# Optimization experiments

Measured on AMD Instinct MI355X. Metric: run time of the kernel, lower is better.

Reference implementation:

```python
import jax, jax.numpy as jnp
import numpy as np
import math

JOINT_DIM = 16
D_MODEL = 128
NUM_HEADS = 8
HEAD_DIM = D_MODEL // NUM_HEADS


def kinematic_adjacency():
    adj = np.zeros((JOINT_DIM, JOINT_DIM), dtype=np.float32)
    skeleton = [(0, 1), (1, 2), (2, 3), (0, 4), (4, 5), (5, 6), (0, 7), (7, 8),
                (8, 9), (0, 10), (10, 11), (11, 12), (0, 13), (13, 14), (14, 15)]
    for p, c in skeleton:
        adj[p, c] = 1.0
        adj[c, p] = 1.0
    sym = [(4, 7), (5, 8), (6, 9), (10, 13), (11, 14), (12, 15)]
    for a, b in sym:
        adj[a, b] += 0.8
        adj[b, a] += 0.8
    adj += np.eye(JOINT_DIM, dtype=np.float32)
    return jnp.asarray(adj)


def setup_inputs() -> dict:
    key = jax.random.key(0)
    ks = jax.random.split(key, 9)
    B, S = 64, 512
    s3 = 1.0 / math.sqrt(3.0)
    sd = 1.0 / math.sqrt(D_MODEL)
    return {
        "x": jax.random.normal(ks[0], (B, S, JOINT_DIM, 3), dtype=jnp.float32),
        "Wq": jax.random.uniform(ks[1], (3, D_MODEL), jnp.float32, -s3, s3),
        "bq": jax.random.uniform(ks[2], (D_MODEL,), jnp.float32, -s3, s3),
        "Wk": jax.random.uniform(ks[3], (3, D_MODEL), jnp.float32, -s3, s3),
        "bk": jax.random.uniform(ks[4], (D_MODEL,), jnp.float32, -s3, s3),
        "Wv": jax.random.uniform(ks[5], (3, D_MODEL), jnp.float32, -s3, s3),
        "bv": jax.random.uniform(ks[6], (D_MODEL,), jnp.float32, -s3, s3),
        "Wo": jax.random.uniform(ks[7], (D_MODEL, D_MODEL), jnp.float32, -sd, sd),
        "bo": jax.random.uniform(ks[8], (D_MODEL,), jnp.float32, -sd, sd),
    }


def reference(x, Wq, bq, Wk, bk, Wv, bv, Wo, bo):
    B, S, J, _ = x.shape
    adj = kinematic_adjacency()  # [J, J]

    def split_heads(t):  # [B,S,J,D] -> [B,S,H,J,hd]
        return t.reshape(B, S, J, NUM_HEADS, HEAD_DIM).transpose(0, 1, 3, 2, 4)

    q = split_heads(x @ Wq + bq)
    k = split_heads(x @ Wk + bk)
    v = split_heads(x @ Wv + bv)

    # scores get adjacency bias BEFORE the 1/sqrt(head_dim) scaling (as in source)
    scores = jnp.einsum('bshjd,bshkd->bshjk', q, k)
    scores = (scores + adj) / math.sqrt(HEAD_DIM)
    w = jax.nn.softmax(scores, axis=-1)  # dropout inactive (eval)
    ctx = jnp.einsum('bshjk,bshkd->bshjd', w, v)
    ctx = ctx.transpose(0, 1, 3, 2, 4).reshape(B, S, J, D_MODEL)
    return ctx @ Wo + bo  # [B,S,J,D]
```

## Files before the change

kernel.cpp:

```cpp
#include <hip/hip_runtime.h>

#define NJ   16
#define DM   128
#define NH   8
#define P    8
#define CL   0.36067376022224085f

typedef __attribute__((ext_vector_type(8))) short bf16x8;
typedef __attribute__((ext_vector_type(4))) float f32x4;

__constant__ float c_adj[NJ * NJ] = {
    1,1,0,0, 1,0,0,1, 0,0,1,0, 0,1,0,0,
    1,1,1,0, 0,0,0,0, 0,0,0,0, 0,0,0,0,
    0,1,1,1, 0,0,0,0, 0,0,0,0, 0,0,0,0,
    0,0,1,1, 0,0,0,0, 0,0,0,0, 0,0,0,0,
    1,0,0,0, 1,1,0,0.8f, 0,0,0,0, 0,0,0,0,
    0,0,0,0, 1,1,1,0, 0.8f,0,0,0, 0,0,0,0,
    0,0,0,0, 0,1,1,0, 0,0.8f,0,0, 0,0,0,0,
    1,0,0,0, 0.8f,0,0,1, 1,0,0,0, 0,0,0,0,
    0,0,0,0, 0,0.8f,0,1, 1,1,0,0, 0,0,0,0,
    0,0,0,0, 0,0,0.8f,0, 1,1,0,0, 0,0,0,0,
    1,0,0,0, 0,0,0,0, 0,0,1,1, 0,0.8f,0,0,
    0,0,0,0, 0,0,0,0, 0,0,1,1, 1,0,0.8f,0,
    0,0,0,0, 0,0,0,0, 0,0,0,1, 1,0,0,0.8f,
    1,0,0,0, 0,0,0,0, 0,0,0.8f,0, 0,1,1,0,
    0,0,0,0, 0,0,0,0, 0,0,0,0.8f, 0,1,1,1,
    0,0,0,0, 0,0,0,0, 0,0,0,0, 0.8f,0,1,1
};

#define WS_BP_W   0
#define WS_PACK_W 128
#define WS_GF_W   256

__device__ __forceinline__ unsigned short f2bf(float f) {
    union { float f; unsigned u; } v; v.f = f;
    unsigned u = v.u;
    u += 0x7FFFu + ((u >> 16) & 1u);
    return (unsigned short)(u >> 16);
}
__device__ __forceinline__ unsigned pack2bf(float lo, float hi) {
    return (unsigned)f2bf(lo) | ((unsigned)f2bf(hi) << 16);
}

__global__ __launch_bounds__(256) void skel_setup_kernel(
    const float* __restrict__ Wq, const float* __restrict__ bq,
    const float* __restrict__ Wk, const float* __restrict__ bk,
    const float* __restrict__ Wv, const float* __restrict__ bv,
    const float* __restrict__ Wo, const float* __restrict__ bo,
    unsigned* __restrict__ wsu)
{
    const int b = blockIdx.x, t = threadIdx.x;
    float* wsf = (float*)wsu;

    if (b < 8) {
        const int idx = b * 256 + t;
        const int ctl = idx >> 2, i = idx & 3;
        const int ct = ctl >> 6, l = ctl & 63;
        const int n  = ct * 16 + (l & 15);
        const int kb = (l >> 4) * 8;
        float v[2];
#pragma unroll
        for (int s = 0; s < 2; ++s) {
            const int k = kb + 2 * i + s;
            const int h = k >> 2, r = k & 3;
            float acc = 0.f;
            if (r < 3) {
#pragma unroll
                for (int dh = 0; dh < 16; ++dh)
                    acc += Wv[r * DM + h * 16 + dh] * Wo[(h * 16 + dh) * DM + n];
            }
            v[s] = acc;
        }
        wsu[WS_GF_W + idx] = pack2bf(v[0], v[1]);
        return;
    }
    if (t < 128) {
        const int n = t;
        float bv_ = bo[n];
        for (int d = 0; d < DM; ++d) bv_ += bv[d] * Wo[d * DM + n];
        wsf[WS_BP_W + n] = bv_;
    } else if (t < 128 + NH) {
        const int h = t - 128;
        float* o = &wsf[WS_PACK_W + h * 16];
#pragma unroll
        for (int r = 0; r < 3; ++r)
#pragma unroll
            for (int c = 0; c < 3; ++c) {
                float acc = 0.f;
#pragma unroll
                for (int dh = 0; dh < 16; ++dh)
                    acc += Wq[r * DM + h * 16 + dh] * Wk[c * DM + h * 16 + dh];
                o[r * 3 + c] = acc * CL;
            }
#pragma unroll
        for (int r = 0; r < 3; ++r) {
            float aa = 0.f, cc = 0.f;
#pragma unroll
            for (int dh = 0; dh < 16; ++dh) {
                aa += Wq[r * DM + h * 16 + dh] * bk[h * 16 + dh];
                cc += Wk[r * DM + h * 16 + dh] * bq[h * 16 + dh];
            }
            o[9 + r]  = aa * CL;
            o[12 + r] = cc * CL;
        }
        float dd = 0.f;
#pragma unroll
        for (int dh = 0; dh < 16; ++dh) dd += bq[h * 16 + dh] * bk[h * 16 + dh];
        o[15] = dd * CL;
    }
}

__global__ __launch_bounds__(256) void skel_main_kernel(
    const float* __restrict__ x,
    const unsigned* __restrict__ wsu,
    float* __restrict__ out,
    int npos)
{
    const int t = threadIdx.x;
    const long pos0 = (long)blockIdx.x * P;
    const float* wsf = (const float*)wsu;

    __shared__ __align__(16) float    sx4[P][NJ][4];
    __shared__ float                  sc[128];
    __shared__ __align__(16) float    st[4][NH][17][4];
    __shared__ __align__(16) unsigned sxb[4][NJ * 16];
    __shared__ __align__(16) unsigned sgf[2048];
    __shared__ __align__(16) float    sbp[128];

    if (t < 128) {
        const int p = t >> 4, j = t & 15;
        const long pidx = pos0 + p;
        const long base = pidx * 48 + j * 3;
        const bool ok = pidx < npos;
        sx4[p][j][0] = ok ? x[base + 0] : 0.f;
        sx4[p][j][1] = ok ? x[base + 1] : 0.f;
        sx4[p][j][2] = ok ? x[base + 2] : 0.f;
        sx4[p][j][3] = 0.f;
    } else {
        const int i = t - 128;
        sc[i]  = wsf[WS_PACK_W + i];
        sbp[i] = wsf[WS_BP_W + i];
    }
    {
        const uint4* gsrc = (const uint4*)&wsu[WS_GF_W];
        uint4* gdst = (uint4*)sgf;
        gdst[t]       = gsrc[t];
        gdst[t + 256] = gsrc[t + 256];
    }
    __syncthreads();

    const int wv = t >> 6, l = t & 63;
    const int h  = l >> 3, j0 = l & 7;

    float m[16];
#pragma unroll
    for (int i = 0; i < 16; ++i) m[i] = sc[h * 16 + i];
    float adj0[NJ], adj1[NJ];
#pragma unroll
    for (int k = 0; k < NJ; ++k) {
        adj0[k] = c_adj[j0 * NJ + k] * CL;
        adj1[k] = c_adj[(j0 + 8) * NJ + k] * CL;
    }

    const int jB = l & 15, lkB = l >> 4;

    for (int it = 0; it < 2; ++it) {
        const int p = wv * 2 + it;

        const f32x4 xa = *(const f32x4*)&sx4[p][j0];
        const f32x4 xb = *(const f32x4*)&sx4[p][j0 + 8];
        {
            f32x4 tv;
            tv.x = m[0]*xa.x + m[1]*xa.y + m[2]*xa.z;
            tv.y = m[3]*xa.x + m[4]*xa.y + m[5]*xa.z;
            tv.z = m[6]*xa.x + m[7]*xa.y + m[8]*xa.z;
            tv.w = m[12]*xa.x + m[13]*xa.y + m[14]*xa.z + m[15];
            *(f32x4*)&st[wv][h][j0][0] = tv;
            tv.x = m[0]*xb.x + m[1]*xb.y + m[2]*xb.z;
            tv.y = m[3]*xb.x + m[4]*xb.y + m[5]*xb.z;
            tv.z = m[6]*xb.x + m[7]*xb.y + m[8]*xb.z;
            tv.w = m[12]*xb.x + m[13]*xb.y + m[14]*xb.z + m[15];
            *(f32x4*)&st[wv][h][j0 + 8][0] = tv;
        }

        const float u0 = m[9]*xa.x + m[10]*xa.y + m[11]*xa.z;
        const float u1 = m[9]*xb.x + m[10]*xb.y + m[11]*xb.z;
        float sum0 = 0.f, sum1 = 0.f;
        float a00 = 0.f, a01 = 0.f, a02 = 0.f;
        float a10 = 0.f, a11 = 0.f, a12 = 0.f;
#pragma unroll
        for (int k = 0; k < NJ; ++k) {
            const f32x4 tk = *(const f32x4*)&st[wv][h][k][0];
            const f32x4 xk = *(const f32x4*)&sx4[p][k];
            const float s0 = xa.x*tk.x + xa.y*tk.y + xa.z*tk.z + (tk.w + u0 + adj0[k]);
            const float s1 = xb.x*tk.x + xb.y*tk.y + xb.z*tk.z + (tk.w + u1 + adj1[k]);
            const float e0 = exp2f(s0);
            const float e1 = exp2f(s1);
            sum0 += e0; sum1 += e1;
            a00 += e0 * xk.x; a01 += e0 * xk.y; a02 += e0 * xk.z;
            a10 += e1 * xk.x; a11 += e1 * xk.y; a12 += e1 * xk.z;
        }
        const float inv0 = __builtin_amdgcn_rcpf(sum0);
        const float inv1 = __builtin_amdgcn_rcpf(sum1);

        {
            uint2 w0, w1;
            w0.x = pack2bf(a00 * inv0, a01 * inv0);
            w0.y = pack2bf(a02 * inv0, 0.f);
            w1.x = pack2bf(a10 * inv1, a11 * inv1);
            w1.y = pack2bf(a12 * inv1, 0.f);
            *(uint2*)&sxb[wv][j0 * 16 + 2 * h]       = w0;
            *(uint2*)&sxb[wv][(j0 + 8) * 16 + 2 * h] = w1;
        }

        if (pos0 + p < npos) {
            const bf16x8 bvec = *(const bf16x8*)&sxb[wv][jB * 16 + lkB * 4];
            float* obase = out + (pos0 + p) * (long)(NJ * DM) + jB * DM + lkB * 4;
#pragma unroll
            for (int ct = 0; ct < 8; ++ct) {
                const bf16x8 ga = *(const bf16x8*)&sgf[(ct * 64 + l) * 4];
                const f32x4 bp4 = *(const f32x4*)&sbp[ct * 16 + lkB * 4];
                f32x4 acc = bp4;
                acc = __builtin_amdgcn_mfma_f32_16x16x32_bf16(ga, bvec, acc, 0, 0, 0);
                *(f32x4*)(obase + ct * 16) = acc;
            }
        }
    }
}

extern "C" void kernel_launch(void* const* d_in, const int* in_sizes, int n_in,
                              void* d_out, int out_size, void* d_ws, size_t ws_size,
                              hipStream_t stream) {
    const float* x  = (const float*)d_in[0];
    const float* Wq = (const float*)d_in[1];
    const float* bq = (const float*)d_in[2];
    const float* Wk = (const float*)d_in[3];
    const float* bk = (const float*)d_in[4];
    const float* Wv = (const float*)d_in[5];
    const float* bv = (const float*)d_in[6];
    const float* Wo = (const float*)d_in[7];
    const float* bo = (const float*)d_in[8];
    float* out    = (float*)d_out;
    unsigned* wsu = (unsigned*)d_ws;

    const int npos = in_sizes[0] / (NJ * 3);
    skel_setup_kernel<<<9, 256, 0, stream>>>(Wq, bq, Wk, bk, Wv, bv, Wo, bo, wsu);
    const int grid = (npos + P - 1) / P;
    skel_main_kernel<<<grid, 256, 0, stream>>>(x, wsu, out, npos);
}
```

Before: 78.66 us.

## Stage MFMA output through swizzled LDS for coalesced stores; keep weights in registers

Each wave now writes its MFMA results into a per-wave LDS tile using an XOR swizzle, then reads them back so each global store covers contiguous 1 KB rows instead of scattered 16-byte fragments. The projected weight fragments move from a per-block LDS copy into registers loaded straight from global memory. The per-head score transform is folded into per-query coefficients instead of going through an LDS staging table. This is meant to improve write coalescing on an output-bandwidth-bound kernel, at the cost of more LDS traffic, extra registers and a larger LDS footprint.

```diff
diff --git a/kernel.cpp b/kernel.cpp
--- a/kernel.cpp
+++ b/kernel.cpp
@@ -122,10 +122,9 @@
 
     __shared__ __align__(16) float    sx4[P][NJ][4];
     __shared__ float                  sc[128];
-    __shared__ __align__(16) float    st[4][NH][17][4];
-    __shared__ __align__(16) unsigned sxb[4][NJ * 16];
-    __shared__ __align__(16) unsigned sgf[2048];
+    __shared__ __align__(16) unsigned sxb[4][NJ * 20];
     __shared__ __align__(16) float    sbp[128];
+    __shared__ __align__(16) float    sout[4][NJ * DM];
 
     if (t < 128) {
         const int p = t >> 4, j = t & 15;
@@ -141,16 +140,16 @@
         sc[i]  = wsf[WS_PACK_W + i];
         sbp[i] = wsf[WS_BP_W + i];
     }
-    {
-        const uint4* gsrc = (const uint4*)&wsu[WS_GF_W];
-        uint4* gdst = (uint4*)sgf;
-        gdst[t]       = gsrc[t];
-        gdst[t + 256] = gsrc[t + 256];
-    }
     __syncthreads();
 
     const int wv = t >> 6, l = t & 63;
     const int h  = l >> 3, j0 = l & 7;
+    const int jB = l & 15, lkB = l >> 4;
+
+    bf16x8 ga[8];
+#pragma unroll
+    for (int ct = 0; ct < 8; ++ct)
+        ga[ct] = *(const bf16x8*)&wsu[WS_GF_W + (ct * 64 + l) * 4];
 
     float m[16];
 #pragma unroll
@@ -162,40 +161,30 @@
         adj1[k] = c_adj[(j0 + 8) * NJ + k] * CL;
     }
 
-    const int jB = l & 15, lkB = l >> 4;
+    float* so = &sout[wv][0];
 
     for (int it = 0; it < 2; ++it) {
         const int p = wv * 2 + it;
-
         const f32x4 xa = *(const f32x4*)&sx4[p][j0];
         const f32x4 xb = *(const f32x4*)&sx4[p][j0 + 8];
-        {
-            f32x4 tv;
-            tv.x = m[0]*xa.x + m[1]*xa.y + m[2]*xa.z;
-            tv.y = m[3]*xa.x + m[4]*xa.y + m[5]*xa.z;
-            tv.z = m[6]*xa.x + m[7]*xa.y + m[8]*xa.z;
-            tv.w = m[12]*xa.x + m[13]*xa.y + m[14]*xa.z + m[15];
-            *(f32x4*)&st[wv][h][j0][0] = tv;
-            tv.x = m[0]*xb.x + m[1]*xb.y + m[2]*xb.z;
-            tv.y = m[3]*xb.x + m[4]*xb.y + m[5]*xb.z;
-            tv.z = m[6]*xb.x + m[7]*xb.y + m[8]*xb.z;
-            tv.w = m[12]*xb.x + m[13]*xb.y + m[14]*xb.z + m[15];
-            *(f32x4*)&st[wv][h][j0 + 8][0] = tv;
-        }
-
-        const float u0 = m[9]*xa.x + m[10]*xa.y + m[11]*xa.z;
-        const float u1 = m[9]*xb.x + m[10]*xb.y + m[11]*xb.z;
+
+        const float y00 = m[0]*xa.x + m[3]*xa.y + m[6]*xa.z + m[12];
+        const float y01 = m[1]*xa.x + m[4]*xa.y + m[7]*xa.z + m[13];
+        const float y02 = m[2]*xa.x + m[5]*xa.y + m[8]*xa.z + m[14];
+        const float u0  = m[9]*xa.x + m[10]*xa.y + m[11]*xa.z + m[15];
+        const float y10 = m[0]*xb.x + m[3]*xb.y + m[6]*xb.z + m[12];
+        const float y11 = m[1]*xb.x + m[4]*xb.y + m[7]*xb.z + m[13];
+        const float y12 = m[2]*xb.x + m[5]*xb.y + m[8]*xb.z + m[14];
+        const float u1  = m[9]*xb.x + m[10]*xb.y + m[11]*xb.z + m[15];
+
         float sum0 = 0.f, sum1 = 0.f;
         float a00 = 0.f, a01 = 0.f, a02 = 0.f;
         float a10 = 0.f, a11 = 0.f, a12 = 0.f;
 #pragma unroll
         for (int k = 0; k < NJ; ++k) {
-            const f32x4 tk = *(const f32x4*)&st[wv][h][k][0];
             const f32x4 xk = *(const f32x4*)&sx4[p][k];
-            const float s0 = xa.x*tk.x + xa.y*tk.y + xa.z*tk.z + (tk.w + u0 + adj0[k]);
-            const float s1 = xb.x*tk.x + xb.y*tk.y + xb.z*tk.z + (tk.w + u1 + adj1[k]);
-            const float e0 = exp2f(s0);
-            const float e1 = exp2f(s1);
+            const float e0 = exp2f(y00*xk.x + y01*xk.y + y02*xk.z + u0 + adj0[k]);
+            const float e1 = exp2f(y10*xk.x + y11*xk.y + y12*xk.z + u1 + adj1[k]);
             sum0 += e0; sum1 += e1;
             a00 += e0 * xk.x; a01 += e0 * xk.y; a02 += e0 * xk.z;
             a10 += e1 * xk.x; a11 += e1 * xk.y; a12 += e1 * xk.z;
@@ -209,20 +198,26 @@
             w0.y = pack2bf(a02 * inv0, 0.f);
             w1.x = pack2bf(a10 * inv1, a11 * inv1);
             w1.y = pack2bf(a12 * inv1, 0.f);
-            *(uint2*)&sxb[wv][j0 * 16 + 2 * h]       = w0;
-            *(uint2*)&sxb[wv][(j0 + 8) * 16 + 2 * h] = w1;
+            *(uint2*)&sxb[wv][j0 * 20 + 2 * h]       = w0;
+            *(uint2*)&sxb[wv][(j0 + 8) * 20 + 2 * h] = w1;
+        }
+        const bf16x8 bvec = *(const bf16x8*)&sxb[wv][jB * 20 + lkB * 4];
+
+#pragma unroll
+        for (int ct = 0; ct < 8; ++ct) {
+            f32x4 acc = *(const f32x4*)&sbp[ct * 16 + lkB * 4];
+            acc = __builtin_amdgcn_mfma_f32_16x16x32_bf16(ga[ct], bvec, acc, 0, 0, 0);
+            *(f32x4*)&so[jB * 128 + (((ct * 4 + lkB) ^ (jB & 7)) << 2)] = acc;
         }
 
         if (pos0 + p < npos) {
-            const bf16x8 bvec = *(const bf16x8*)&sxb[wv][jB * 16 + lkB * 4];
-            float* obase = out + (pos0 + p) * (long)(NJ * DM) + jB * DM + lkB * 4;
-#pragma unroll
-            for (int ct = 0; ct < 8; ++ct) {
-                const bf16x8 ga = *(const bf16x8*)&sgf[(ct * 64 + l) * 4];
-                const f32x4 bp4 = *(const f32x4*)&sbp[ct * 16 + lkB * 4];
-                f32x4 acc = bp4;
-                acc = __builtin_amdgcn_mfma_f32_16x16x32_bf16(ga, bvec, acc, 0, 0, 0);
-                *(f32x4*)(obase + ct * 16) = acc;
+            float* ob = out + (pos0 + p) * (long)(NJ * DM);
+#pragma unroll
+            for (int c2 = 0; c2 < 8; ++c2) {
+                const int jR = c2 * 2 + (l >> 5);
+                const int ul = l & 31;
+                const f32x4 vq = *(const f32x4*)&so[jR * 128 + ((ul ^ (jR & 7)) << 2)];
+                *(f32x4*)(ob + c2 * 256 + l * 4) = vq;
             }
         }
     }
```

Result: faster. 66.26 us (-15.8%).
